# Performance work log

Measured on AMD Instinct MI355X. Metric: run time of the kernel, lower is better.

Reference implementation:

```python
import jax, jax.numpy as jnp
import numpy as np

ROPE_BASE = 100.0


def _rope1d(tok, pos):
    # tok: [B, H, N, d], pos: [B, N] int. Matches croco apply_rope1d.
    d = tok.shape[-1]
    inv_freq = 1.0 / (ROPE_BASE ** (jnp.arange(0, d, 2, dtype=jnp.float32) / d))  # [d/2]
    ang = pos[:, None, :, None].astype(jnp.float32) * inv_freq  # [B,1,N,d/2]
    ang = jnp.concatenate([ang, ang], axis=-1)  # [B,1,N,d]
    cos, sin = jnp.cos(ang).astype(tok.dtype), jnp.sin(ang).astype(tok.dtype)
    x1, x2 = tok[..., : d // 2], tok[..., d // 2 :]
    rot = jnp.concatenate([-x2, x1], axis=-1)  # rotate_half
    return tok * cos + rot * sin


def _rope2d(tok, pos):
    # tok: [B, H, N, D]; first half of D uses pos[...,0] (y), second half pos[...,1] (x)
    y, x = jnp.split(tok, 2, axis=-1)
    return jnp.concatenate([_rope1d(y, pos[..., 0]), _rope1d(x, pos[..., 1])], axis=-1)


def setup_inputs() -> dict:
    key = jax.random.key(0)
    ks = jax.random.split(key, 10)
    B, N, C = 8, 1024, 768
    s = 0.02
    return {
        "query": jax.random.normal(ks[0], (B, N, C), jnp.float32),
        "key": jax.random.normal(ks[1], (B, N, C), jnp.float32),
        "value": jax.random.normal(ks[2], (B, N, C), jnp.float32),
        "qpos": jax.random.randint(ks[3], (B, N, 2), 0, 32, jnp.int32),
        "kpos": jax.random.randint(ks[4], (B, N, 2), 0, 32, jnp.int32),
        "Wq": jax.random.normal(ks[5], (C, C), jnp.float32) * s,
        "Wk": jax.random.normal(ks[6], (C, C), jnp.float32) * s,
        "Wv": jax.random.normal(ks[7], (C, C), jnp.float32) * s,
        "Wo": jax.random.normal(ks[8], (C, C), jnp.float32) * s,
        "bo": jnp.zeros((C,), jnp.float32),
    }


def reference(query, key, value, qpos, kpos, Wq, Wk, Wv, Wo, bo):
    B, Nq, C = query.shape
    H = 12
    hd = C // H
    scale = hd ** -0.5
    # projections (torch Linear: x @ W^T), then split heads -> [B,H,N,hd]
    q = jnp.einsum("bnc,dc->bnd", query, Wq).reshape(B, Nq, H, hd).transpose(0, 2, 1, 3)
    k = jnp.einsum("bnc,dc->bnd", key, Wk).reshape(B, -1, H, hd).transpose(0, 2, 1, 3)
    v = jnp.einsum("bnc,dc->bnd", value, Wv).reshape(B, -1, H, hd).transpose(0, 2, 1, 3)
    q = _rope2d(q, qpos)
    k = _rope2d(k, kpos)
    attn = jnp.einsum("bhqd,bhkd->bhqk", q, k) * scale
    attn = jax.nn.softmax(attn, axis=-1)
    x = jnp.einsum("bhqk,bhkd->bhqd", attn, v)
    x = x.transpose(0, 2, 1, 3).reshape(B, Nq, C)
    return jnp.einsum("bnc,dc->bnd", x, Wo) + bo
```

## Files before the change

kernel.cpp:

```cpp
#include <hip/hip_runtime.h>
#include <hip/hip_bf16.h>
#include <hip/hip_fp16.h>

#define B_DIM 8
#define N_DIM 1024
#define C_DIM 768
#define H_DIM 12
#define HD    64
#define M_DIM (B_DIM * N_DIM)
#define BH    (B_DIM * H_DIM)

static constexpr size_t TEN = (size_t)M_DIM * C_DIM;
static constexpr size_t WN  = (size_t)C_DIM * C_DIM;

typedef __attribute__((ext_vector_type(8))) short    s16x8;
typedef __attribute__((ext_vector_type(8))) _Float16 f16x8;
typedef __attribute__((ext_vector_type(4))) float    f32x4;

__device__ __forceinline__ unsigned short f2h(float f) {
    __half h = __float2half(f);
    return __half_as_ushort(h);
}


__global__ __launch_bounds__(256)
void convX(const float* __restrict__ q, const float* __restrict__ k,
           const float* __restrict__ v, unsigned short* __restrict__ XS)
{
    const int t  = blockIdx.z;
    const int p  = blockIdx.y;
    const int kb = blockIdx.x;
    const float* src = (t == 0) ? q : (t == 1 ? k : v);
    unsigned short* dst = XS + (size_t)t * TEN;

    const int mr = threadIdx.x & 127;
    const int gh = threadIdx.x >> 7;
    const float* s = src + ((size_t)(p * 128 + mr)) * C_DIM + kb * 32 + gh * 16;
    float4 v0 = *(const float4*)(s);
    float4 v1 = *(const float4*)(s + 4);
    float4 v2 = *(const float4*)(s + 8);
    float4 v3 = *(const float4*)(s + 12);
    float f[16] = {v0.x,v0.y,v0.z,v0.w, v1.x,v1.y,v1.z,v1.w,
                   v2.x,v2.y,v2.z,v2.w, v3.x,v3.y,v3.z,v3.w};
    #pragma unroll
    for (int gj = 0; gj < 2; ++gj) {
        int gg = gh * 2 + gj;
        s16x8 h8;
        #pragma unroll
        for (int e = 0; e < 8; ++e)
            h8[e] = (short)f2h(f[gj * 8 + e]);
        size_t a = ((((size_t)p * 24 + kb) * 4 + gg) * 128 + mr) * 8;
        *(s16x8*)(dst + a) = h8;
    }
}

__global__ __launch_bounds__(256)
void convW(const float* __restrict__ wq, const float* __restrict__ wk,
           const float* __restrict__ wv, const float* __restrict__ wo,
           unsigned short* __restrict__ WS, float2* __restrict__ tab)
{
    if (blockIdx.x == 0 && blockIdx.y == 0 && blockIdx.z == 0) {
        #pragma unroll
        for (int i = 0; i < 2; ++i) {
            int t = threadIdx.x + i * 256;
            int pos = t >> 4, j = t & 15;
            float ang = (float)pos * exp2f(-(float)j * 0.41524101186092029f);
            float s, c;
            sincosf(ang, &s, &c);
            tab[t] = make_float2(c, s);
        }
    }

    const int t  = blockIdx.z;
    const int p  = blockIdx.y;
    const int kb = blockIdx.x;
    const float* src = (t == 0) ? wq : (t == 1 ? wk : (t == 2 ? wv : wo));
    unsigned short* dst = WS + (size_t)t * WN;

    const int mr = threadIdx.x & 127;
    const int gh = threadIdx.x >> 7;
    const float* s = src + ((size_t)(p * 128 + mr)) * C_DIM + kb * 32 + gh * 16;
    float4 v0 = *(const float4*)(s);
    float4 v1 = *(const float4*)(s + 4);
    float4 v2 = *(const float4*)(s + 8);
    float4 v3 = *(const float4*)(s + 12);
    float f[16] = {v0.x,v0.y,v0.z,v0.w, v1.x,v1.y,v1.z,v1.w,
                   v2.x,v2.y,v2.z,v2.w, v3.x,v3.y,v3.z,v3.w};
    #pragma unroll
    for (int gj = 0; gj < 2; ++gj) {
        int gg = gh * 2 + gj;
        s16x8 h8;
        #pragma unroll
        for (int e = 0; e < 8; ++e)
            h8[e] = (short)f2h(f[gj * 8 + e]);
        size_t a = ((((size_t)p * 24 + kb) * 4 + gg) * 128 + mr) * 8;
        *(s16x8*)(dst + a) = h8;
    }
}

template<int MODE>
__global__ __launch_bounds__(256)
void gemmF(const unsigned short* __restrict__ XQ, const unsigned short* __restrict__ XK,
           const unsigned short* __restrict__ XV,
           const unsigned short* __restrict__ WQ, const unsigned short* __restrict__ WK,
           const unsigned short* __restrict__ WV,
           const int* __restrict__ qpos, const int* __restrict__ kpos,
           const float2* __restrict__ tab,
           unsigned short* __restrict__ OQ, unsigned short* __restrict__ OK_,
           unsigned short* __restrict__ OV,
           const float* __restrict__ bias, float* __restrict__ Of)
{
    extern __shared__ unsigned short smem_us[];
    auto sA = reinterpret_cast<unsigned short (*)[4][128][8]>(smem_us);

    const int tid  = threadIdx.x;
    const int lane = tid & 63;
    const int w    = tid >> 6;
    const int wr   = w >> 1, wc = w & 1;
    const int c    = lane & 15, g = lane >> 4;

    const int chunk = gridDim.x >> 3;
    const int wgid  = (blockIdx.x & 7) * chunk + (blockIdx.x >> 3);
    int z, m0, n0;
    if (MODE == 1) {
        z = wgid / 384;
        int r = wgid - z * 384;
        m0 = (r / 6) * 128;
        n0 = (r % 6) * 128;
    } else {
        z = 0;
        m0 = (wgid / 12) * 128;
        n0 = (wgid % 12) * 64;
    }

    const unsigned short *Ap, *Bp;
    if (MODE == 0 || z == 0) { Ap = XQ; Bp = WQ; }
    else if (z == 1)         { Ap = XK; Bp = WK; }
    else                     { Ap = XV; Bp = WV; }

    const size_t abase0 = (size_t)(m0 >> 7) * 24 * 4096;
    const size_t bbase0 = (size_t)(n0 >> 7) * 24 * 4096;

    if constexpr (MODE == 1) {
        auto sB = reinterpret_cast<unsigned short (*)[4][128][8]>(smem_us + 8192);

        f32x4 acc[4][4] = {};

        auto stage = [&](int kb, int buf) {
            #pragma unroll
            for (int t = 0; t < 4; ++t) {
                int is = w * 4 + t;
                int sel = is >> 3;
                int j   = is & 7;
                int gg  = j >> 1, half = j & 1;
                const unsigned short* srcp =
                    (sel ? Bp + bbase0 : Ap + abase0) + (size_t)kb * 4096
                    + (size_t)gg * 1024 + (half * 64 + lane) * 8;
                unsigned short* dstp = sel ? &sB[buf][gg][half * 64][0]
                                           : &sA[buf][gg][half * 64][0];
                __builtin_amdgcn_global_load_lds(
                    (const __attribute__((address_space(1))) void*)srcp,
                    (__attribute__((address_space(3))) void*)dstp,
                    16, 0, 0);
            }
        };

        stage(0, 0);
        stage(1, 1);

        for (int kb = 0; kb < 24; ++kb) {
            int buf = kb & 1;
            if (kb < 23) asm volatile("s_waitcnt vmcnt(4)" ::: "memory");
            else         asm volatile("s_waitcnt vmcnt(0)" ::: "memory");
            __builtin_amdgcn_sched_barrier(0);
            __builtin_amdgcn_s_barrier();
            __builtin_amdgcn_sched_barrier(0);

            f16x8 a[4], b[4];
            #pragma unroll
            for (int mi = 0; mi < 4; ++mi)
                a[mi] = *(const f16x8*)&sA[buf][g][wr * 64 + 16 * mi + c][0];
            #pragma unroll
            for (int ni = 0; ni < 4; ++ni)
                b[ni] = *(const f16x8*)&sB[buf][g][wc * 64 + 16 * ni + c][0];
            __builtin_amdgcn_s_setprio(1);
            #pragma unroll
            for (int mi = 0; mi < 4; ++mi)
                #pragma unroll
                for (int ni = 0; ni < 4; ++ni)
                    acc[mi][ni] = __builtin_amdgcn_mfma_f32_16x16x32_f16(a[mi], b[ni], acc[mi][ni], 0, 0, 0);
            __builtin_amdgcn_s_setprio(0);

            __builtin_amdgcn_sched_barrier(0);
            __builtin_amdgcn_s_barrier();
            __builtin_amdgcn_sched_barrier(0);
            if (kb + 2 < 24) stage(kb + 2, buf);
        }

        if (z == 2) {
            __syncthreads();
            auto T = reinterpret_cast<unsigned short (*)[132]>(smem_us);
            #pragma unroll
            for (int ni = 0; ni < 4; ++ni) {
                int dl = wc * 64 + 16 * ni + c;
                #pragma unroll
                for (int mi = 0; mi < 4; ++mi) {
                    int ml = wr * 64 + 16 * mi + 4 * g;
                    unsigned short hs[4];
                    #pragma unroll
                    for (int r = 0; r < 4; ++r)
                        hs[r] = f2h(acc[mi][ni][r]);
                    *(uint2*)&T[dl][ml] =
                        make_uint2((unsigned)hs[0] | ((unsigned)hs[1] << 16),
                                   (unsigned)hs[2] | ((unsigned)hs[3] << 16));
                }
            }
            __syncthreads();
            const int b = m0 >> 10, nbase = m0 & 1023;
            #pragma unroll
            for (int it = 0; it < 8; ++it) {
                int f  = tid + it * 256;
                int dl = f >> 4;
                int mc = (f & 15) * 8;
                s16x8 vv = *(const s16x8*)&T[dl][mc];
                int d = n0 + dl, h = d >> 6, dh = d & 63;
                *(s16x8*)(OV + ((size_t)(b * H_DIM + h) * HD + dh) * N_DIM + nbase + mc) = vv;
            }
        } else {
            const int* P = z ? kpos : qpos;
            unsigned short* T = z ? OK_ : OQ;
            const float scale = z ? 1.0f : 0.18033688011112042f;
            const int hh = (n0 >> 6) + wc;
            #pragma unroll
            for (int mi = 0; mi < 4; ++mi)
                #pragma unroll
                for (int r = 0; r < 4; ++r) {
                    int m = m0 + wr * 64 + 16 * mi + 4 * g + r;
                    int b = m >> 10, n = m & 1023;
                    size_t base = ((size_t)(b * H_DIM + hh) * N_DIM + n) * HD;
                    #pragma unroll
                    for (int bb = 0; bb < 2; ++bb) {
                        int pos = P[2 * m + bb];
                        float2 cs = tab[pos * 16 + c];
                        float x1 = acc[mi][bb * 2 + 0][r];
                        float x2 = acc[mi][bb * 2 + 1][r];
                        float r1 = (x1 * cs.x - x2 * cs.y) * scale;
                        float r2 = (x2 * cs.x + x1 * cs.y) * scale;
                        T[base + bb * 32 + c]      = f2h(r1);
                        T[base + bb * 32 + 16 + c] = f2h(r2);
                    }
                }
        }
    } else {
        auto sB = reinterpret_cast<unsigned short (*)[4][64][8]>(smem_us + 8192);
        const int r0 = n0 & 127;

        f32x4 acc[4][2] = {};

        auto stage = [&](int kb, int buf) {
            #pragma unroll
            for (int t = 0; t < 3; ++t) {
                int is = w * 3 + t;
                if (is < 8) {
                    int gg = is & 3, half = is >> 2;
                    const unsigned short* srcp = Ap + abase0 + (size_t)kb * 4096
                        + (size_t)gg * 1024 + (half * 64 + lane) * 8;
                    __builtin_amdgcn_global_load_lds(
                        (const __attribute__((address_space(1))) void*)srcp,
                        (__attribute__((address_space(3))) void*)&sA[buf][gg][half * 64][0],
                        16, 0, 0);
                } else {
                    int gg = is - 8;
                    const unsigned short* srcp = Bp + bbase0 + (size_t)kb * 4096
                        + (size_t)gg * 1024 + (r0 + lane) * 8;
                    __builtin_amdgcn_global_load_lds(
                        (const __attribute__((address_space(1))) void*)srcp,
                        (__attribute__((address_space(3))) void*)&sB[buf][gg][0][0],
                        16, 0, 0);
                }
            }
        };

        stage(0, 0);
        stage(1, 1);

        for (int kb = 0; kb < 24; ++kb) {
            int buf = kb & 1;
            if (kb < 23) asm volatile("s_waitcnt vmcnt(3)" ::: "memory");
            else         asm volatile("s_waitcnt vmcnt(0)" ::: "memory");
            __builtin_amdgcn_sched_barrier(0);
            __builtin_amdgcn_s_barrier();
            __builtin_amdgcn_sched_barrier(0);

            f16x8 a[4], b[2];
            #pragma unroll
            for (int mi = 0; mi < 4; ++mi)
                a[mi] = *(const f16x8*)&sA[buf][g][wr * 64 + 16 * mi + c][0];
            #pragma unroll
            for (int ni = 0; ni < 2; ++ni)
                b[ni] = *(const f16x8*)&sB[buf][g][wc * 32 + 16 * ni + c][0];
            __builtin_amdgcn_s_setprio(1);
            #pragma unroll
            for (int mi = 0; mi < 4; ++mi)
                #pragma unroll
                for (int ni = 0; ni < 2; ++ni)
                    acc[mi][ni] = __builtin_amdgcn_mfma_f32_16x16x32_f16(a[mi], b[ni], acc[mi][ni], 0, 0, 0);
            __builtin_amdgcn_s_setprio(0);

            __builtin_amdgcn_sched_barrier(0);
            __builtin_amdgcn_s_barrier();
            __builtin_amdgcn_sched_barrier(0);
            if (kb + 2 < 24) stage(kb + 2, buf);
        }

        #pragma unroll
        for (int ni = 0; ni < 2; ++ni) {
            int d = n0 + wc * 32 + 16 * ni + c;
            float bv = bias[d];
            #pragma unroll
            for (int mi = 0; mi < 4; ++mi)
                #pragma unroll
                for (int r = 0; r < 4; ++r) {
                    int m = m0 + wr * 64 + 16 * mi + 4 * g + r;
                    Of[(size_t)m * C_DIM + d] = acc[mi][ni][r] + bv;
                }
        }
    }
}

__global__ __launch_bounds__(256)
void attn_f16(const unsigned short* __restrict__ Qh, const unsigned short* __restrict__ Kh,
              const unsigned short* __restrict__ Vt,
              unsigned short* __restrict__ Xb)
{
    __shared__ _Float16 sK[64][72];
    __shared__ _Float16 sV[64][72];
    __shared__ _Float16 sP[4][2][16][72];

    const int tid  = threadIdx.x;
    const int lane = tid & 63;
    const int wv   = tid >> 6;
    const int c    = lane & 15;
    const int g    = lane >> 4;

    const int bid   = blockIdx.x;
    const int xcd   = bid & 7;
    const int local = bid >> 3;
    const int bh    = xcd * 12 + (local >> 3);
    const int q0    = (local & 7) * 128;
    const size_t hb = (size_t)bh * (N_DIM * HD);

    const size_t qoffA = hb + (size_t)(q0 + wv * 32 + c) * HD;
    const size_t qoffB = qoffA + (size_t)16 * HD;
    f16x8 qA0 = *(const f16x8*)(Qh + qoffA + 8 * g);
    f16x8 qA1 = *(const f16x8*)(Qh + qoffA + 32 + 8 * g);
    f16x8 qB0 = *(const f16x8*)(Qh + qoffB + 8 * g);
    f16x8 qB1 = *(const f16x8*)(Qh + qoffB + 32 + 8 * g);

    f16x8 ones;
    #pragma unroll
    for (int e = 0; e < 8; ++e) ones[e] = (_Float16)1.0f;

    f32x4 accA[4] = {}, accB[4] = {};
    f32x4 lAcc[2] = {};

    const int f0 = tid, f1 = tid + 256;
    const int row0 = f0 >> 3, ch0 = (f0 & 7) * 8;
    const int row1 = f1 >> 3, ch1 = (f1 & 7) * 8;
    const unsigned short* Kbase = Kh + hb;
    const unsigned short* Vbase = Vt + hb;

    s16x8 rK0 = *(const s16x8*)(Kbase + (size_t)row0 * HD + ch0);
    s16x8 rK1 = *(const s16x8*)(Kbase + (size_t)row1 * HD + ch1);
    s16x8 rV0 = *(const s16x8*)(Vbase + (size_t)row0 * N_DIM + ch0);
    s16x8 rV1 = *(const s16x8*)(Vbase + (size_t)row1 * N_DIM + ch1);

    for (int kt = 0; kt < 16; ++kt) {
        __builtin_amdgcn_s_barrier();

        *(s16x8*)&sK[row0][ch0] = rK0;
        *(s16x8*)&sK[row1][ch1] = rK1;
        *(s16x8*)&sV[row0][ch0] = rV0;
        *(s16x8*)&sV[row1][ch1] = rV1;

        if (kt < 15) {
            rK0 = *(const s16x8*)(Kbase + (size_t)((kt + 1) * 64 + row0) * HD + ch0);
            rK1 = *(const s16x8*)(Kbase + (size_t)((kt + 1) * 64 + row1) * HD + ch1);
            rV0 = *(const s16x8*)(Vbase + (size_t)row0 * N_DIM + (kt + 1) * 64 + ch0);
            rV1 = *(const s16x8*)(Vbase + (size_t)row1 * N_DIM + (kt + 1) * 64 + ch1);
        }

        asm volatile("s_waitcnt lgkmcnt(0)" ::: "memory");
        __builtin_amdgcn_sched_barrier(0);
        __builtin_amdgcn_s_barrier();
        __builtin_amdgcn_sched_barrier(0);

        f32x4 sA[4] = {}, sB[4] = {};
        __builtin_amdgcn_s_setprio(1);
        #pragma unroll
        for (int st = 0; st < 4; ++st) {
            f16x8 a0 = *(const f16x8*)&sK[16 * st + c][8 * g];
            f16x8 a1 = *(const f16x8*)&sK[16 * st + c][32 + 8 * g];
            sA[st] = __builtin_amdgcn_mfma_f32_16x16x32_f16(a0, qA0, sA[st], 0, 0, 0);
            sA[st] = __builtin_amdgcn_mfma_f32_16x16x32_f16(a1, qA1, sA[st], 0, 0, 0);
            sB[st] = __builtin_amdgcn_mfma_f32_16x16x32_f16(a0, qB0, sB[st], 0, 0, 0);
            sB[st] = __builtin_amdgcn_mfma_f32_16x16x32_f16(a1, qB1, sB[st], 0, 0, 0);
        }
        __builtin_amdgcn_s_setprio(0);

        #pragma unroll
        for (int st = 0; st < 4; ++st) {
            float pA[4], pB[4];
            #pragma unroll
            for (int r = 0; r < 4; ++r) {
                pA[r] = __builtin_amdgcn_exp2f(sA[st][r]);
                pB[r] = __builtin_amdgcn_exp2f(sB[st][r]);
            }
            __half2 a01 = __float22half2_rn(make_float2(pA[0], pA[1]));
            __half2 a23 = __float22half2_rn(make_float2(pA[2], pA[3]));
            __half2 b01 = __float22half2_rn(make_float2(pB[0], pB[1]));
            __half2 b23 = __float22half2_rn(make_float2(pB[2], pB[3]));
            *(uint2*)&sP[wv][0][c][16 * st + 4 * g] =
                make_uint2(*(unsigned*)&a01, *(unsigned*)&a23);
            *(uint2*)&sP[wv][1][c][16 * st + 4 * g] =
                make_uint2(*(unsigned*)&b01, *(unsigned*)&b23);
        }

        __builtin_amdgcn_s_setprio(1);
        #pragma unroll
        for (int m = 0; m < 2; ++m) {
            f16x8 pbA = *(const f16x8*)&sP[wv][0][c][32 * m + 8 * g];
            f16x8 pbB = *(const f16x8*)&sP[wv][1][c][32 * m + 8 * g];
            #pragma unroll
            for (int sd = 0; sd < 4; ++sd) {
                f16x8 va = *(const f16x8*)&sV[16 * sd + c][32 * m + 8 * g];
                accA[sd] = __builtin_amdgcn_mfma_f32_16x16x32_f16(va, pbA, accA[sd], 0, 0, 0);
                accB[sd] = __builtin_amdgcn_mfma_f32_16x16x32_f16(va, pbB, accB[sd], 0, 0, 0);
            }
            lAcc[0] = __builtin_amdgcn_mfma_f32_16x16x32_f16(ones, pbA, lAcc[0], 0, 0, 0);
            lAcc[1] = __builtin_amdgcn_mfma_f32_16x16x32_f16(ones, pbB, lAcc[1], 0, 0, 0);
        }
        __builtin_amdgcn_s_setprio(0);
    }

    float invA = 1.0f / lAcc[0][0];
    float invB = 1.0f / lAcc[1][0];

    const int b = bh / H_DIM, h = bh % H_DIM;
    #pragma unroll
    for (int sub = 0; sub < 2; ++sub) {
        const f32x4* acc = sub ? accB : accA;
        float invl = sub ? invB : invA;
        const int q = q0 + wv * 32 + sub * 16 + c;
        const int m  = b * N_DIM + q;
        const int p_ = m >> 7, mr = m & 127;
        #pragma unroll
        for (int sd = 0; sd < 4; ++sd) {
            int kdim = h * 64 + 16 * sd + 4 * g;
            int kb = kdim >> 5;
            int gg = (kdim >> 3) & 3;
            int e  = kdim & 7;
            size_t a = ((((size_t)p_ * 24 + kb) * 4 + gg) * 128 + mr) * 8 + e;
            unsigned short hs[4];
            #pragma unroll
            for (int r = 0; r < 4; ++r)
                hs[r] = f2h(acc[sd][r] * invl);
            *(uint2*)(Xb + a) =
                make_uint2((unsigned)hs[0] | ((unsigned)hs[1] << 16),
                           (unsigned)hs[2] | ((unsigned)hs[3] << 16));
        }
    }
}

extern "C" void kernel_launch(void* const* d_in, const int* in_sizes, int n_in,
                              void* d_out, int out_size, void* d_ws, size_t ws_size,
                              hipStream_t stream)
{
    const float* query = (const float*)d_in[0];
    const float* key_  = (const float*)d_in[1];
    const float* value = (const float*)d_in[2];
    const int*   qpos  = (const int*)d_in[3];
    const int*   kpos  = (const int*)d_in[4];
    const float* Wq    = (const float*)d_in[5];
    const float* Wk    = (const float*)d_in[6];
    const float* Wv    = (const float*)d_in[7];
    const float* Wo    = (const float*)d_in[8];
    const float* bo    = (const float*)d_in[9];
    float* out = (float*)d_out;

    unsigned short* XS  = (unsigned short*)d_ws;
    unsigned short* WS  = XS + 3 * TEN;
    unsigned short* Qh  = WS + 4 * WN;
    unsigned short* Kh  = Qh + TEN;
    unsigned short* Vt  = Kh + TEN;
    unsigned short* Xb  = Vt + TEN;
    float2* tab = (float2*)(Xb + TEN);

    convX<<<dim3(24, 64, 3), 256, 0, stream>>>(query, key_, value, XS);
    convW<<<dim3(24, 6, 4), 256, 0, stream>>>(Wq, Wk, Wv, Wo, WS, tab);

    gemmF<1><<<dim3(1152), 256, 33792, stream>>>(
        XS + 0 * TEN, XS + 1 * TEN, XS + 2 * TEN,
        WS + 0 * WN, WS + 1 * WN, WS + 2 * WN,
        qpos, kpos, tab, Qh, Kh, Vt, nullptr, nullptr);

    attn_f16<<<dim3(768), 256, 0, stream>>>(Qh, Kh, Vt, Xb);

    gemmF<0><<<dim3(768), 256, 24576, stream>>>(
        Xb, nullptr, nullptr,
        WS + 3 * WN, nullptr, nullptr,
        nullptr, nullptr, nullptr, nullptr, nullptr, nullptr, bo, out);
}
```

Baseline: 131.3 us.

## Merge input/weight conversion kernels and restructure GEMM double-buffer pipeline

Measured after the change: 138.5 us. 5.5% more time.

```diff
diff --git a/kernel.cpp b/kernel.cpp
--- a/kernel.cpp
+++ b/kernel.cpp
@@ -24,18 +24,47 @@
 
 
 __global__ __launch_bounds__(256)
-void convX(const float* __restrict__ q, const float* __restrict__ k,
-           const float* __restrict__ v, unsigned short* __restrict__ XS)
+void convAll(const float* __restrict__ q, const float* __restrict__ k,
+             const float* __restrict__ v,
+             const float* __restrict__ wq, const float* __restrict__ wk,
+             const float* __restrict__ wv, const float* __restrict__ wo,
+             unsigned short* __restrict__ XS, unsigned short* __restrict__ WS,
+             float2* __restrict__ tab)
 {
-    const int t  = blockIdx.z;
+    const int z  = blockIdx.z;
     const int p  = blockIdx.y;
     const int kb = blockIdx.x;
-    const float* src = (t == 0) ? q : (t == 1 ? k : v);
-    unsigned short* dst = XS + (size_t)t * TEN;
+
+    if (z == 3 && p == 0 && kb == 0) {
+        #pragma unroll
+        for (int i = 0; i < 2; ++i) {
+            int t = threadIdx.x + i * 256;
+            int pos = t >> 4, j = t & 15;
+            float ang = (float)pos * exp2f(-(float)j * 0.41524101186092029f);
+            float s, c;
+            sincosf(ang, &s, &c);
+            tab[t] = make_float2(c, s);
+        }
+    }
+
+    const float* src;
+    unsigned short* dst;
+    int panel;
+    if (z < 3) {
+        src = (z == 0) ? q : (z == 1 ? k : v);
+        dst = XS + (size_t)z * TEN;
+        panel = p;
+    } else {
+        if (p >= 24) return;
+        int t = p / 6;
+        src = (t == 0) ? wq : (t == 1 ? wk : (t == 2 ? wv : wo));
+        dst = WS + (size_t)t * WN;
+        panel = p % 6;
+    }
 
     const int mr = threadIdx.x & 127;
     const int gh = threadIdx.x >> 7;
-    const float* s = src + ((size_t)(p * 128 + mr)) * C_DIM + kb * 32 + gh * 16;
+    const float* s = src + ((size_t)(panel * 128 + mr)) * C_DIM + kb * 32 + gh * 16;
     float4 v0 = *(const float4*)(s);
     float4 v1 = *(const float4*)(s + 4);
     float4 v2 = *(const float4*)(s + 8);
@@ -49,51 +78,7 @@
         #pragma unroll
         for (int e = 0; e < 8; ++e)
             h8[e] = (short)f2h(f[gj * 8 + e]);
-        size_t a = ((((size_t)p * 24 + kb) * 4 + gg) * 128 + mr) * 8;
-        *(s16x8*)(dst + a) = h8;
-    }
-}
-
-__global__ __launch_bounds__(256)
-void convW(const float* __restrict__ wq, const float* __restrict__ wk,
-           const float* __restrict__ wv, const float* __restrict__ wo,
-           unsigned short* __restrict__ WS, float2* __restrict__ tab)
-{
-    if (blockIdx.x == 0 && blockIdx.y == 0 && blockIdx.z == 0) {
-        #pragma unroll
-        for (int i = 0; i < 2; ++i) {
-            int t = threadIdx.x + i * 256;
-            int pos = t >> 4, j = t & 15;
-            float ang = (float)pos * exp2f(-(float)j * 0.41524101186092029f);
-            float s, c;
-            sincosf(ang, &s, &c);
-            tab[t] = make_float2(c, s);
-        }
-    }
-
-    const int t  = blockIdx.z;
-    const int p  = blockIdx.y;
-    const int kb = blockIdx.x;
-    const float* src = (t == 0) ? wq : (t == 1 ? wk : (t == 2 ? wv : wo));
-    unsigned short* dst = WS + (size_t)t * WN;
-
-    const int mr = threadIdx.x & 127;
-    const int gh = threadIdx.x >> 7;
-    const float* s = src + ((size_t)(p * 128 + mr)) * C_DIM + kb * 32 + gh * 16;
-    float4 v0 = *(const float4*)(s);
-    float4 v1 = *(const float4*)(s + 4);
-    float4 v2 = *(const float4*)(s + 8);
-    float4 v3 = *(const float4*)(s + 12);
-    float f[16] = {v0.x,v0.y,v0.z,v0.w, v1.x,v1.y,v1.z,v1.w,
-                   v2.x,v2.y,v2.z,v2.w, v3.x,v3.y,v3.z,v3.w};
-    #pragma unroll
-    for (int gj = 0; gj < 2; ++gj) {
-        int gg = gh * 2 + gj;
-        s16x8 h8;
-        #pragma unroll
-        for (int e = 0; e < 8; ++e)
-            h8[e] = (short)f2h(f[gj * 8 + e]);
-        size_t a = ((((size_t)p * 24 + kb) * 4 + gg) * 128 + mr) * 8;
+        size_t a = ((((size_t)panel * 24 + kb) * 4 + gg) * 128 + mr) * 8;
         *(s16x8*)(dst + a) = h8;
     }
 }
@@ -166,15 +151,14 @@
         };
 
         stage(0, 0);
-        stage(1, 1);
+        asm volatile("s_waitcnt vmcnt(0)" ::: "memory");
+        __builtin_amdgcn_sched_barrier(0);
+        __builtin_amdgcn_s_barrier();
+        __builtin_amdgcn_sched_barrier(0);
 
         for (int kb = 0; kb < 24; ++kb) {
             int buf = kb & 1;
-            if (kb < 23) asm volatile("s_waitcnt vmcnt(4)" ::: "memory");
-            else         asm volatile("s_waitcnt vmcnt(0)" ::: "memory");
-            __builtin_amdgcn_sched_barrier(0);
-            __builtin_amdgcn_s_barrier();
-            __builtin_amdgcn_sched_barrier(0);
+            if (kb + 1 < 24) stage(kb + 1, buf ^ 1);
 
             f16x8 a[4], b[4];
             #pragma unroll
@@ -191,10 +175,10 @@
                     acc[mi][ni] = __builtin_amdgcn_mfma_f32_16x16x32_f16(a[mi], b[ni], acc[mi][ni], 0, 0, 0);
             __builtin_amdgcn_s_setprio(0);
 
+            asm volatile("s_waitcnt vmcnt(0)" ::: "memory");
             __builtin_amdgcn_sched_barrier(0);
             __builtin_amdgcn_s_barrier();
             __builtin_amdgcn_sched_barrier(0);
-            if (kb + 2 < 24) stage(kb + 2, buf);
         }
 
         if (z == 2) {
@@ -496,8 +480,8 @@
     unsigned short* Xb  = Vt + TEN;
     float2* tab = (float2*)(Xb + TEN);
 
-    convX<<<dim3(24, 64, 3), 256, 0, stream>>>(query, key_, value, XS);
-    convW<<<dim3(24, 6, 4), 256, 0, stream>>>(Wq, Wk, Wv, Wo, WS, tab);
+    convAll<<<dim3(24, 64, 4), 256, 0, stream>>>(
+        query, key_, value, Wq, Wk, Wv, Wo, XS, WS, tab);
 
     gemmF<1><<<dim3(1152), 256, 33792, stream>>>(
         XS + 0 * TEN, XS + 1 * TEN, XS + 2 * TEN,
```
